# Kernel optimization log

Measured on AMD Instinct MI355X. Metric: run time of the kernel, lower is better.

Reference implementation:

```python
import jax, jax.numpy as jnp
import numpy as np

N_NODES = 100000
BN_EPS = 1e-5


def _linear_params(key, fan_in, fan_out):
    k1, k2 = jax.random.split(key)
    lim = 1.0 / np.sqrt(fan_in)
    W = jax.random.uniform(k1, (fan_in, fan_out), jnp.float32, -lim, lim)
    b = jax.random.uniform(k2, (fan_out,), jnp.float32, -lim, lim)
    return W, b


def setup_inputs() -> dict:
    key = jax.random.key(0)
    ks = jax.random.split(key, 24)
    in_ch, hid, tdim, L = 17, 64, 32, 2
    E = 1600000
    inp = {}
    inp["x"] = jax.random.normal(ks[0], (N_NODES, in_ch), jnp.float32)
    inp["edge_index"] = jax.random.randint(ks[1], (2, E), 0, N_NODES, jnp.int64)
    inp["edge_dts"] = jax.random.uniform(ks[2], (E,), jnp.float32) * 100.0
    inp["batch_size"] = 10000
    # TimeEncode params (learned, TGAT init)
    inp["basis_freq"] = jnp.asarray(1.0 / 10 ** np.linspace(0, 9, tdim), jnp.float32)
    inp["phase"] = jnp.zeros((tdim,), jnp.float32)
    # TMP edge MLP: in = 2*in_ch + tdim
    mi = 2 * in_ch + tdim
    inp["tmp_W1"], inp["tmp_b1"] = _linear_params(ks[3], mi, mi // 2)
    inp["tmp_W2"], inp["tmp_b2"] = _linear_params(ks[4], mi // 2, in_ch)
    inp["proj_W"], inp["proj_b"] = _linear_params(ks[5], in_ch, hid)
    # SMP layers (stacked over L)
    si = 2 * hid
    W1s, b1s, W2s, b2s = [], [], [], []
    for l in range(L):
        W1, b1 = _linear_params(ks[6 + 2 * l], si, si // 2)
        W2, b2 = _linear_params(ks[7 + 2 * l], si // 2, hid)
        W1s.append(W1); b1s.append(b1); W2s.append(W2); b2s.append(b2)
    inp["smp_W1"] = jnp.stack(W1s); inp["smp_b1"] = jnp.stack(b1s)
    inp["smp_W2"] = jnp.stack(W2s); inp["smp_b2"] = jnp.stack(b2s)
    inp["bn_gamma"] = jnp.ones((L, hid), jnp.float32)
    inp["bn_beta"] = jnp.zeros((L, hid), jnp.float32)
    # classifier head
    inp["clf_W1"], inp["clf_b1"] = _linear_params(ks[12], hid, hid)
    inp["clf_g1"] = jnp.ones((hid,), jnp.float32); inp["clf_bb1"] = jnp.zeros((hid,), jnp.float32)
    inp["clf_W2"], inp["clf_b2"] = _linear_params(ks[13], hid, hid // 2)
    inp["clf_g2"] = jnp.ones((hid // 2,), jnp.float32); inp["clf_bb2"] = jnp.zeros((hid // 2,), jnp.float32)
    inp["clf_W3"], inp["clf_b3"] = _linear_params(ks[14], hid // 2, 1)
    return inp


def _segment_mean(vals, idx, n):
    s = jax.ops.segment_sum(vals, idx, num_segments=n)
    c = jax.ops.segment_sum(jnp.ones((idx.shape[0], 1), vals.dtype), idx, num_segments=n)
    return s / jnp.maximum(c, 1.0)


def _bn(x, g, b):
    m = x.mean(0)
    v = x.var(0)
    return (x - m) * jax.lax.rsqrt(v + BN_EPS) * g + b


def reference(x, edge_index, edge_dts, batch_size, basis_freq, phase,
              tmp_W1, tmp_b1, tmp_W2, tmp_b2, proj_W, proj_b,
              smp_W1, smp_b1, smp_W2, smp_b2, bn_gamma, bn_beta,
              clf_W1, clf_b1, clf_g1, clf_bb1,
              clf_W2, clf_b2, clf_g2, clf_bb2, clf_W3, clf_b3):
    src, dst = edge_index[0], edge_index[1]  # x_j = x[src], x_i = x[dst]
    n = x.shape[0]
    # TimeEncode: cos(t * freq + phase)  -> [E, time_dim]
    rel = jnp.cos(edge_dts[:, None] * basis_freq + phase)
    # --- TMP conv (applied once) ---
    x_i = x[dst]
    m_in = jnp.concatenate([x_i, x[src], rel], axis=-1)
    p = jnp.tanh(jax.nn.relu(m_in @ tmp_W1 + tmp_b1) @ tmp_W2 + tmp_b2)
    msg = (2.0 * p - 1.0) * x_i  # (p - q) * x_i with q = 1 - p
    h = x + _segment_mean(msg, dst, n)
    # --- project to hidden ---
    h = h @ proj_W + proj_b
    # --- L SMP layers with BatchNorm + ReLU (dropout = eval/identity) ---
    L = smp_W1.shape[0]
    for l in range(L):
        h_i = h[dst]
        m_in = jnp.concatenate([h_i, h[src]], axis=-1)
        p = jnp.tanh(jax.nn.relu(m_in @ smp_W1[l] + smp_b1[l]) @ smp_W2[l] + smp_b2[l])
        h = h + _segment_mean((2.0 * p - 1.0) * h_i, dst, n)
        h = jax.nn.relu(_bn(h, bn_gamma[l], bn_beta[l]))
    # --- classifier on seed nodes ---
    z = h[:batch_size]
    z = jax.nn.relu(_bn(z @ clf_W1 + clf_b1, clf_g1, clf_bb1))
    z = jax.nn.relu(_bn(z @ clf_W2 + clf_b2, clf_g2, clf_bb2))
    return z @ clf_W3 + clf_b3  # [batch_size, 1] logits
```

## Files before the change

kernel.cpp:

```cpp
#include <hip/hip_runtime.h>
#include <hip/hip_bf16.h>


typedef float  f32x4 __attribute__((ext_vector_type(4)));
typedef short  s16x8 __attribute__((ext_vector_type(8)));

__device__ __forceinline__ float tanh_factor(float u) {
  float e = __expf(2.0f * u);
  return fmaf(-4.0f, __builtin_amdgcn_rcpf(e + 1.0f), 1.0f);
}

__device__ __forceinline__ void atomic_add_f32(float* p, float v) {
  unsafeAtomicAdd(p, v);
}

__device__ __forceinline__ unsigned short f2bf(float f) {
  __hip_bfloat16 b = __float2bfloat16(f);
  return *(unsigned short*)&b;
}
__device__ __forceinline__ float bf2f(unsigned short u) {
  unsigned int v = ((unsigned int)u) << 16;
  return *(float*)&v;
}

__global__ __launch_bounds__(256) void k_hist(
    const int* __restrict__ ei, int* __restrict__ cntI, int E)
{
  int e = blockIdx.x * 256 + threadIdx.x;
  if (e < E) atomicAdd(&cntI[__builtin_nontemporal_load(ei + E + e)], 1);
}

__global__ __launch_bounds__(256) void k_scan_block(
    const int* __restrict__ cntI, int* __restrict__ cursor,
    int* __restrict__ bsum, int N)
{
  __shared__ int s[256];
  const int t = threadIdx.x;
  int i = blockIdx.x * 256 + t;
  int v = (i < N) ? cntI[i] : 0;
  s[t] = v;
  for (int off = 1; off < 256; off <<= 1) {
    __syncthreads();
    int x = (t >= off) ? s[t - off] : 0;
    __syncthreads();
    s[t] += x;
  }
  __syncthreads();
  if (i < N) cursor[i] = s[t] - v;
  if (t == 255) bsum[blockIdx.x] = s[255];
}

__global__ __launch_bounds__(512) void k_scan_bsum(int* __restrict__ bsum, int nb)
{
  __shared__ int s[512];
  const int t = threadIdx.x;
  int v = (t < nb) ? bsum[t] : 0;
  s[t] = v;
  for (int off = 1; off < 512; off <<= 1) {
    __syncthreads();
    int x = (t >= off) ? s[t - off] : 0;
    __syncthreads();
    s[t] += x;
  }
  __syncthreads();
  if (t < nb) bsum[t] = s[t] - v;
}

__global__ __launch_bounds__(256) void k_expand_add(
    int* __restrict__ cursor, const int* __restrict__ bsum,
    const int* __restrict__ cntI, int* __restrict__ dstS, int N)
{
  int n = blockIdx.x * 256 + threadIdx.x;
  if (n >= N) return;
  int cur = cursor[n] + bsum[blockIdx.x];
  cursor[n] = cur;
  int c = cntI[n];
  for (int i = 0; i < c; i++) dstS[cur + i] = n;
}

__global__ __launch_bounds__(256) void k_scatter_x(
    const int* __restrict__ ei, const float* __restrict__ dts,
    int* __restrict__ cursor, int2* __restrict__ srcdtS, int E, int N)
{
  const int g  = blockIdx.x & 7;
  const int bi = blockIdx.x >> 3;
  const int nb = gridDim.x >> 3;
  const int lo = (int)(((long long)N * g) >> 3);
  const int hi = (int)(((long long)N * (g + 1)) >> 3);
  for (int e = bi * 256 + threadIdx.x; e < E; e += nb * 256) {
    int d = __builtin_nontemporal_load(ei + E + e);
    if (d >= lo && d < hi) {
      int s = __builtin_nontemporal_load(ei + e);
      float dt = __builtin_nontemporal_load(dts + e);
      int pos = atomicAdd(&cursor[d], 1);
      srcdtS[pos] = make_int2(s, __float_as_int(dt));
    }
  }
}

__global__ __launch_bounds__(256) void prep_all(
    const float* __restrict__ x, const float* __restrict__ tW1,
    const float* __restrict__ tW2, const float* __restrict__ sW1,
    const float* __restrict__ sW2, const float* __restrict__ cW1,
    const float* __restrict__ cW2, unsigned short* __restrict__ xb,
    unsigned short* __restrict__ W1t1, unsigned short* __restrict__ W2t1,
    unsigned short* __restrict__ W1t, unsigned short* __restrict__ W2t,
    unsigned short* __restrict__ cW1t, unsigned short* __restrict__ cW2t, int N)
{
  int i = blockIdx.x * 256 + threadIdx.x;
  int totalX = N * 24;
  for (int idx = i; idx < totalX; idx += gridDim.x * 256) {
    int n = idx / 24, c = idx - n * 24;
    xb[idx] = (c < 17) ? f2bf(x[n * 17 + c]) : (unsigned short)0;
  }
  if (i < 48 * 96) {
    int n = i / 96, k = i - n * 96;
    int src = (k < 17) ? k : (k >= 24 && k < 41) ? (k - 24 + 17)
            : (k >= 48 && k < 80) ? (k - 48 + 34) : -1;
    W1t1[i] = (n < 33 && src >= 0) ? f2bf(tW1[src * 33 + n]) : (unsigned short)0;
  }
  if (i < 32 * 64) {
    int n = i / 64, k = i - n * 64;
    W2t1[i] = (n < 17 && k < 33) ? f2bf(tW2[k * 17 + n]) : (unsigned short)0;
  }
  if (i < 2 * 64 * 128) {
    int l = i >> 13; int r = i & 8191; int n = r >> 7; int k = r & 127;
    W1t[i] = f2bf(sW1[((size_t)l * 128 + k) * 64 + n]);
  }
  if (i < 2 * 64 * 64) {
    int l = i >> 12; int r = i & 4095; int n = r >> 6; int k = r & 63;
    W2t[i] = f2bf(sW2[((size_t)l * 64 + k) * 64 + n]);
  }
  if (i < 64 * 64) {
    int c = i >> 6, k = i & 63;
    cW1t[i] = f2bf(cW1[k * 64 + c]);
  }
  if (i < 32 * 64) {
    int c = i >> 6, k = i & 63;
    cW2t[i] = f2bf(cW2[k * 32 + c]);
  }
}

__global__ __launch_bounds__(256, 3) void phase1_edge_mfma(
    const unsigned short* __restrict__ xb, const int* __restrict__ dstS,
    const int2* __restrict__ srcdtS, const float* __restrict__ freq,
    const float* __restrict__ phs,
    const unsigned short* __restrict__ W1t1, const float* __restrict__ b1,
    const unsigned short* __restrict__ W2t1, const float* __restrict__ b2,
    float* __restrict__ accum, int E, int nwt)
{
  __shared__ unsigned short sA[64][104];
  __shared__ unsigned short sHid[64][72];
  __shared__ float sRed[64][20];
  __shared__ int   sDst[64];

  const int t = threadIdx.x;
  const int wv = t >> 6, lane = t & 63, l16 = lane & 15, quad = lane >> 4;
  const int r0 = wv * 16;

  s16x8 w1f[3][3], w2f[2][2];
  float bias1[3], bias2[2];
#pragma unroll
  for (int cb = 0; cb < 3; cb++) {
    int n = cb * 16 + l16;
#pragma unroll
    for (int kb = 0; kb < 3; kb++)
      w1f[cb][kb] = *(const s16x8*)&W1t1[n * 96 + kb * 32 + quad * 8];
    bias1[cb] = (n < 33) ? b1[n] : 0.0f;
  }
#pragma unroll
  for (int cb = 0; cb < 2; cb++) {
    int n = cb * 16 + l16;
#pragma unroll
    for (int kb = 0; kb < 2; kb++)
      w2f[cb][kb] = *(const s16x8*)&W2t1[n * 64 + kb * 32 + quad * 8];
    bias2[cb] = (n < 17) ? b2[n] : 0.0f;
  }

  for (int i = lane; i < 16 * 28; i += 64) {
    int rr = r0 + i / 28, c = i % 28;
    int col = (c < 6) ? 18 + c : (c < 12) ? 42 + (c - 6) : 80 + (c - 12);
    sA[rr][col] = 0;
  }
  for (int i = lane; i < 256; i += 64)
    sHid[r0 + (i >> 4)][48 + (i & 15)] = 0;

  const int gw = blockIdx.x * 4 + wv;
  const int nw = gridDim.x * 4;

  const int e_loc = lane >> 2, q = lane & 3;
  const int rr = r0 + e_loc;

  int ndP = 0; uint4 xa0, xa1; unsigned int xa2 = 0; float dtP = 0.0f;
  auto issue = [&](int tt) {
    int er = (tt << 4) + e_loc; if (er >= E) er = E - 1;
    if (q < 2) {
      ndP = q ? srcdtS[er].x : dstS[er];
      const unsigned short* src = &xb[(size_t)ndP * 24];
      xa0 = *(const uint4*)&src[0];
      xa1 = *(const uint4*)&src[8];
      xa2 = *(const unsigned int*)&src[16];
    } else {
      dtP = __int_as_float(srcdtS[er].y);
    }
  };
  issue(gw < nwt ? gw : 0);

  for (int tile = gw; tile < nwt; tile += nw) {
    const int eb = tile << 4;

    if (q < 2) {
      if (!q) sDst[rr] = ndP;
      const int base = q ? 24 : 0;
      *(uint4*)&sA[rr][base]     = xa0;
      *(uint4*)&sA[rr][base + 8] = xa1;
      *(unsigned int*)&sA[rr][base + 16] = xa2;
    } else {
      const int k0 = (q == 2) ? 0 : 16;
      unsigned short tmp[16] __attribute__((aligned(16)));
#pragma unroll
      for (int j = 0; j < 16; j++)
        tmp[j] = f2bf(__cosf(fmaf(dtP, freq[k0 + j], phs[k0 + j])));
      *(uint4*)&sA[rr][48 + k0]     = *(const uint4*)&tmp[0];
      *(uint4*)&sA[rr][48 + k0 + 8] = *(const uint4*)&tmp[8];
    }

    { int nt = tile + nw; issue(nt < nwt ? nt : tile); }

    f32x4 a1[3];
#pragma unroll
    for (int cb = 0; cb < 3; cb++)
      a1[cb] = (f32x4){bias1[cb], bias1[cb], bias1[cb], bias1[cb]};
#pragma unroll
    for (int kb = 0; kb < 3; kb++) {
      s16x8 aF = *(const s16x8*)&sA[r0 + l16][kb * 32 + quad * 8];
#pragma unroll
      for (int cb = 0; cb < 3; cb++)
        a1[cb] = __builtin_amdgcn_mfma_f32_16x16x32_bf16(aF, w1f[cb][kb], a1[cb], 0, 0, 0);
    }
#pragma unroll
    for (int cb = 0; cb < 3; cb++)
#pragma unroll
      for (int reg = 0; reg < 4; reg++)
        sHid[r0 + quad * 4 + reg][cb * 16 + l16] = f2bf(fmaxf(a1[cb][reg], 0.0f));

    f32x4 a2[2];
#pragma unroll
    for (int cb = 0; cb < 2; cb++)
      a2[cb] = (f32x4){bias2[cb], bias2[cb], bias2[cb], bias2[cb]};
#pragma unroll
    for (int kb = 0; kb < 2; kb++) {
      s16x8 aF = *(const s16x8*)&sHid[r0 + l16][kb * 32 + quad * 8];
#pragma unroll
      for (int cb = 0; cb < 2; cb++)
        a2[cb] = __builtin_amdgcn_mfma_f32_16x16x32_bf16(aF, w2f[cb][kb], a2[cb], 0, 0, 0);
    }

#pragma unroll
    for (int reg = 0; reg < 4; reg++) {
      int row = r0 + quad * 4 + reg;
      bool ok = (eb + quad * 4 + reg < E);
      sRed[row][l16] = ok ? tanh_factor(a2[0][reg]) : 0.0f;
      if (l16 == 0) sRed[row][16] = ok ? tanh_factor(a2[1][reg]) : 0.0f;
    }

    if (lane < 17) {
      int col = lane;
      float run = 0.0f;
      int cur = __builtin_amdgcn_readfirstlane(sDst[r0]);
#pragma unroll
      for (int k = 0; k < 16; k++) {
        int d = __builtin_amdgcn_readfirstlane(sDst[r0 + k]);
        float v = sRed[r0 + k][col];
        if (d != cur) {
          atomic_add_f32(&accum[(size_t)cur * 17 + col], run);
          run = 0.0f; cur = d;
        }
        run += v;
      }
      atomic_add_f32(&accum[(size_t)cur * 17 + col], run);
    }
  }
}

__global__ __launch_bounds__(256) void phase1_node(
    const float* __restrict__ x, const float* __restrict__ acc1,
    const int* __restrict__ cntI, const float* __restrict__ Wp,
    const float* __restrict__ bp, float* __restrict__ h,
    float* __restrict__ acc2, int N)
{
  __shared__ float s0[4][20];
  const int t = threadIdx.x;
  const int nb = blockIdx.x << 2;
  if (t < 68) {
    int nl = t / 17, c = t % 17;
    int n = nb + nl;
    float v = 0.0f;
    if (n < N) {
      float cnt = fmaxf((float)cntI[n], 1.0f);
      v = x[n * 17 + c] * (1.0f + acc1[n * 17 + c] / cnt);
    }
    s0[nl][c] = v;
  }
  __syncthreads();
  int nl = t >> 6, j = t & 63;
  int n = nb + nl;
  if (n < N) {
    float acc = bp[j];
#pragma unroll
    for (int c = 0; c < 17; c++) acc = fmaf(s0[nl][c], Wp[c * 64 + j], acc);
    h[n * 64 + j] = acc;
    acc2[n * 64 + j] = 0.0f;
  }
}

template <bool DO_BN>
__global__ void prep_P(
    float* __restrict__ h, const unsigned short* __restrict__ W1t,
    const float* __restrict__ b1,
    const float* __restrict__ bns, const float* __restrict__ bnq,
    const float* __restrict__ gam, const float* __restrict__ bet, float invR,
    unsigned short* __restrict__ P1, unsigned short* __restrict__ P2, int N)
{
  __shared__ unsigned short sH[64][72];
  __shared__ float sM[64], sS[64], sB[64];
  const int t = threadIdx.x;
  const int wv = t >> 6, lane = t & 63, l16 = lane & 15, quad = lane >> 4;
  const int nb = blockIdx.x << 6;

  if (DO_BN) {
    if (t < 64) {
      float m = bns[t] * invR;
      float var = bnq[t] * invR - m * m;
      sM[t] = m;
      sS[t] = gam[t] * rsqrtf(var + 1e-5f);
      sB[t] = bet[t];
    }
    __syncthreads();
  }

#pragma unroll
  for (int i = 0; i < 4; i++) {
    int g = t + i * 256;
    int r = g >> 4, c4 = (g & 15) << 2;
    int n0 = nb + r;
    bool valid = (n0 < N);
    int n = valid ? n0 : N - 1;
    float4 v = *(const float4*)&h[(size_t)n * 64 + c4];
    if (DO_BN) {
      v.x = fmaxf(fmaf(v.x - sM[c4 + 0], sS[c4 + 0], sB[c4 + 0]), 0.0f);
      v.y = fmaxf(fmaf(v.y - sM[c4 + 1], sS[c4 + 1], sB[c4 + 1]), 0.0f);
      v.z = fmaxf(fmaf(v.z - sM[c4 + 2], sS[c4 + 2], sB[c4 + 2]), 0.0f);
      v.w = fmaxf(fmaf(v.w - sM[c4 + 3], sS[c4 + 3], sB[c4 + 3]), 0.0f);
      if (valid) *(float4*)&h[(size_t)n0 * 64 + c4] = v;
    }
    ushort4 o = { f2bf(v.x), f2bf(v.y), f2bf(v.z), f2bf(v.w) };
    *(ushort4*)&sH[r][c4] = o;
  }
  __syncthreads();

  const int n = nb + wv * 16 + l16;
#pragma unroll
  for (int half = 0; half < 2; half++) {
    f32x4 acc[4];
#pragma unroll
    for (int cb = 0; cb < 4; cb++) {
      if (half == 0) {
        float4 bv = *(const float4*)&b1[cb * 16 + quad * 4];
        acc[cb] = (f32x4){bv.x, bv.y, bv.z, bv.w};
      } else {
        acc[cb] = (f32x4){0.0f, 0.0f, 0.0f, 0.0f};
      }
    }
#pragma unroll
    for (int kb = 0; kb < 2; kb++) {
      s16x8 bF = *(const s16x8*)&sH[wv * 16 + l16][kb * 32 + quad * 8];
#pragma unroll
      for (int cb = 0; cb < 4; cb++) {
        s16x8 aF = *(const s16x8*)&W1t[(cb * 16 + l16) * 128 + half * 64 + kb * 32 + quad * 8];
        acc[cb] = __builtin_amdgcn_mfma_f32_16x16x32_bf16(aF, bF, acc[cb], 0, 0, 0);
      }
    }
    if (n < N) {
      unsigned short* P = half ? P2 : P1;
#pragma unroll
      for (int cb = 0; cb < 4; cb++) {
        ushort4 o = { f2bf(acc[cb][0]), f2bf(acc[cb][1]),
                      f2bf(acc[cb][2]), f2bf(acc[cb][3]) };
        *(ushort4*)&P[(size_t)n * 64 + cb * 16 + quad * 4] = o;
      }
    }
  }
}

__global__ __launch_bounds__(256, 4) void phase2_edge(
    const unsigned short* __restrict__ P1, const unsigned short* __restrict__ P2,
    const int* __restrict__ dstS, const int2* __restrict__ srcdtS,
    const unsigned short* __restrict__ W2t, const float* __restrict__ b2,
    float* __restrict__ accum, int E, int nwt)
{
  __shared__ unsigned short sA[64][136];
  __shared__ int sDst[64];
  float* sRedF = (float*)&sA[0][0];

  const int t = threadIdx.x;
  const int wv = t >> 6, lane = t & 63, l16 = lane & 15, quad = lane >> 4;
  const int r0 = wv * 16;

  s16x8 w2f[4][2];
  f32x4 bias2v[4];
#pragma unroll
  for (int cb = 0; cb < 4; cb++) {
#pragma unroll
    for (int kb = 0; kb < 2; kb++)
      w2f[cb][kb] = *(const s16x8*)&W2t[(cb * 16 + l16) * 64 + kb * 32 + quad * 8];
    float4 bv = *(const float4*)&b2[cb * 16 + quad * 4];
    bias2v[cb] = (f32x4){bv.x, bv.y, bv.z, bv.w};
  }

  const int gw = blockIdx.x * 4 + wv;
  const int nw = gridDim.x * 4;
  const int eRow = r0 + l16;

  const int e_loc = lane >> 2, q = lane & 3;
  const int rr = r0 + e_loc;
  const unsigned short* const Pb = (q < 2) ? P1 : P2;
  const int cb0 = q * 32;
  const size_t sub = (size_t)((q & 1) * 32);

  int ndP = 0; uint4 pA, pB, pC, pD;
  auto issue = [&](int tt) {
    int er = (tt << 4) + e_loc; if (er >= E) er = E - 1;
    ndP = (q < 2) ? dstS[er] : srcdtS[er].x;
    const unsigned short* src = Pb + (size_t)ndP * 64 + sub;
    pA = *(const uint4*)&src[0];
    pB = *(const uint4*)&src[8];
    pC = *(const uint4*)&src[16];
    pD = *(const uint4*)&src[24];
  };
  issue(gw < nwt ? gw : 0);

  for (int tile = gw; tile < nwt; tile += nw) {
    const int eb = tile << 4;

    if (q == 0) sDst[rr] = ndP;
    *(uint4*)&sA[rr][cb0]      = pA;
    *(uint4*)&sA[rr][cb0 + 8]  = pB;
    *(uint4*)&sA[rr][cb0 + 16] = pC;
    *(uint4*)&sA[rr][cb0 + 24] = pD;

    { int nt = tile + nw; issue(nt < nwt ? nt : tile); }

    s16x8 hidf[2];
#pragma unroll
    for (int kb = 0; kb < 2; kb++) {
      s16x8 x1 = *(const s16x8*)&sA[eRow][kb * 32 + quad * 8];
      s16x8 x2 = *(const s16x8*)&sA[eRow][64 + kb * 32 + quad * 8];
      s16x8 hf;
#pragma unroll
      for (int j = 0; j < 8; j++) {
        float a = bf2f((unsigned short)x1[j]);
        float b = bf2f((unsigned short)x2[j]);
        hf[j] = (short)f2bf(fmaxf(a + b, 0.0f));
      }
      hidf[kb] = hf;
    }

    f32x4 acc[4];
#pragma unroll
    for (int cb = 0; cb < 4; cb++) acc[cb] = bias2v[cb];
#pragma unroll
    for (int kb = 0; kb < 2; kb++)
#pragma unroll
      for (int cb = 0; cb < 4; cb++)
        acc[cb] = __builtin_amdgcn_mfma_f32_16x16x32_bf16(w2f[cb][kb], hidf[kb], acc[cb], 0, 0, 0);

    bool ok = (eb + l16 < E);
#pragma unroll
    for (int cb = 0; cb < 4; cb++) {
      f32x4 f;
#pragma unroll
      for (int reg = 0; reg < 4; reg++)
        f[reg] = ok ? tanh_factor(acc[cb][reg]) : 0.0f;
      *(f32x4*)&sRedF[eRow * 68 + cb * 16 + quad * 4] = f;
    }

    {
      float run = 0.0f;
      int cur = __builtin_amdgcn_readfirstlane(sDst[r0]);
#pragma unroll
      for (int k = 0; k < 16; k++) {
        int d = __builtin_amdgcn_readfirstlane(sDst[r0 + k]);
        float v = sRedF[(r0 + k) * 68 + lane];
        if (d != cur) {
          atomic_add_f32(&accum[(size_t)cur * 64 + lane], run);
          run = 0.0f; cur = d;
        }
        run += v;
      }
      atomic_add_f32(&accum[(size_t)cur * 64 + lane], run);
    }
  }
}

__global__ __launch_bounds__(256) void node_update_bn(
    float* __restrict__ h, float* __restrict__ accum,
    const int* __restrict__ cntI, float* __restrict__ bns,
    float* __restrict__ bnq, int N)
{
  const int t = threadIdx.x;
  float ls = 0.0f, lq = 0.0f;
  int total = N * 64;
  for (int idx = blockIdx.x * 256 + t; idx < total; idx += gridDim.x * 256) {
    int n = idx >> 6;
    float cnt = fmaxf((float)cntI[n], 1.0f);
    float v = h[idx] * (1.0f + accum[idx] / cnt);
    accum[idx] = 0.0f;
    h[idx] = v;
    ls += v; lq += v * v;
  }
  __shared__ float ss[256], sq[256];
  ss[t] = ls; sq[t] = lq;
  __syncthreads();
  if (t < 64) {
    float s = ss[t] + ss[t + 64] + ss[t + 128] + ss[t + 192];
    float q = sq[t] + sq[t + 64] + sq[t + 128] + sq[t + 192];
    atomic_add_f32(&bns[t], s);
    atomic_add_f32(&bnq[t], q);
  }
}

template <int NCB>
__global__ __launch_bounds__(256) void clf_mfma(
    const float* __restrict__ in, const unsigned short* __restrict__ Wt,
    const float* __restrict__ bias, float* __restrict__ z,
    float* __restrict__ bns, float* __restrict__ bnq,
    const float* __restrict__ ibns, const float* __restrict__ ibnq,
    const float* __restrict__ igam, const float* __restrict__ ibet,
    float iinvR, int rows)
{
  __shared__ unsigned short sIn[64][72];
  __shared__ float sM[64], sS[64], sB[64];
  const int t = threadIdx.x;
  const int wv = t >> 6, lane = t & 63, l16 = lane & 15, quad = lane >> 4;
  const int nb = blockIdx.x << 6;

  if (t < 64) {
    float m = ibns[t] * iinvR;
    float var = ibnq[t] * iinvR - m * m;
    sM[t] = m;
    sS[t] = igam[t] * rsqrtf(var + 1e-5f);
    sB[t] = ibet[t];
  }

  s16x8 wf[NCB][2];
  f32x4 bv[NCB];
#pragma unroll
  for (int cb = 0; cb < NCB; cb++) {
#pragma unroll
    for (int kb = 0; kb < 2; kb++)
      wf[cb][kb] = *(const s16x8*)&Wt[(cb * 16 + l16) * 64 + kb * 32 + quad * 8];
    float4 b4 = *(const float4*)&bias[cb * 16 + quad * 4];
    bv[cb] = (f32x4){b4.x, b4.y, b4.z, b4.w};
  }
  __syncthreads();

#pragma unroll
  for (int i = 0; i < 4; i++) {
    int g = t + i * 256;
    int r = g >> 4, c4 = (g & 15) << 2;
    int n = nb + r; if (n >= rows) n = rows - 1;
    float4 v = *(const float4*)&in[(size_t)n * 64 + c4];
    v.x = fmaxf(fmaf(v.x - sM[c4 + 0], sS[c4 + 0], sB[c4 + 0]), 0.0f);
    v.y = fmaxf(fmaf(v.y - sM[c4 + 1], sS[c4 + 1], sB[c4 + 1]), 0.0f);
    v.z = fmaxf(fmaf(v.z - sM[c4 + 2], sS[c4 + 2], sB[c4 + 2]), 0.0f);
    v.w = fmaxf(fmaf(v.w - sM[c4 + 3], sS[c4 + 3], sB[c4 + 3]), 0.0f);
    ushort4 o = { f2bf(v.x), f2bf(v.y), f2bf(v.z), f2bf(v.w) };
    *(ushort4*)&sIn[r][c4] = o;
  }
  __syncthreads();

  const int n = nb + wv * 16 + l16;
  const bool ok = (n < rows);
  f32x4 acc[NCB];
#pragma unroll
  for (int cb = 0; cb < NCB; cb++) acc[cb] = bv[cb];
#pragma unroll
  for (int kb = 0; kb < 2; kb++) {
    s16x8 bF = *(const s16x8*)&sIn[wv * 16 + l16][kb * 32 + quad * 8];
#pragma unroll
    for (int cb = 0; cb < NCB; cb++)
      acc[cb] = __builtin_amdgcn_mfma_f32_16x16x32_bf16(wf[cb][kb], bF, acc[cb], 0, 0, 0);
  }

#pragma unroll
  for (int cb = 0; cb < NCB; cb++) {
    if (ok)
      *(float4*)&z[(size_t)n * (NCB * 16) + cb * 16 + quad * 4] =
          make_float4(acc[cb][0], acc[cb][1], acc[cb][2], acc[cb][3]);
    f32x4 s, q;
#pragma unroll
    for (int reg = 0; reg < 4; reg++) {
      float v = ok ? acc[cb][reg] : 0.0f;
      s[reg] = v; q[reg] = v * v;
    }
#pragma unroll
    for (int m = 1; m < 16; m <<= 1) {
#pragma unroll
      for (int reg = 0; reg < 4; reg++) {
        s[reg] += __shfl_xor(s[reg], m);
        q[reg] += __shfl_xor(q[reg], m);
      }
    }
    if (l16 == 0) {
#pragma unroll
      for (int reg = 0; reg < 4; reg++) {
        int col = cb * 16 + quad * 4 + reg;
        atomic_add_f32(&bns[col], s[reg]);
        atomic_add_f32(&bnq[col], q[reg]);
      }
    }
  }
}

__global__ __launch_bounds__(256) void clf_final(
    const float* __restrict__ z2, const float* __restrict__ W3,
    const float* __restrict__ b3,
    const float* __restrict__ ibns, const float* __restrict__ ibnq,
    const float* __restrict__ igam, const float* __restrict__ ibet,
    float iinvR, float* __restrict__ out, int rows)
{
  __shared__ float sM[32], sS[32], sB[32];
  const int t = threadIdx.x;
  if (t < 32) {
    float m = ibns[t] * iinvR;
    float var = ibnq[t] * iinvR - m * m;
    sM[t] = m;
    sS[t] = igam[t] * rsqrtf(var + 1e-5f);
    sB[t] = ibet[t];
  }
  __syncthreads();
  int n = blockIdx.x * 256 + t;
  if (n >= rows) return;
  float acc = b3[0];
#pragma unroll
  for (int k = 0; k < 32; k++) {
    float v = fmaxf(fmaf(z2[n * 32 + k] - sM[k], sS[k], sB[k]), 0.0f);
    acc = fmaf(v, W3[k], acc);
  }
  out[n] = acc;
}

extern "C" void kernel_launch(void* const* d_in, const int* in_sizes, int n_in,
                              void* d_out, int out_size, void* d_ws, size_t ws_size,
                              hipStream_t stream)
{
  const float* x    = (const float*)d_in[0];
  const int*   ei   = (const int*)  d_in[1];
  const float* dts  = (const float*)d_in[2];
  const float* freq = (const float*)d_in[4];
  const float* phs  = (const float*)d_in[5];
  const float* tW1  = (const float*)d_in[6];
  const float* tb1  = (const float*)d_in[7];
  const float* tW2  = (const float*)d_in[8];
  const float* tb2  = (const float*)d_in[9];
  const float* pW   = (const float*)d_in[10];
  const float* pb   = (const float*)d_in[11];
  const float* sW1  = (const float*)d_in[12];
  const float* sb1  = (const float*)d_in[13];
  const float* sW2  = (const float*)d_in[14];
  const float* sb2  = (const float*)d_in[15];
  const float* bng  = (const float*)d_in[16];
  const float* bnb  = (const float*)d_in[17];
  const float* cW1  = (const float*)d_in[18];
  const float* cb1  = (const float*)d_in[19];
  const float* cg1  = (const float*)d_in[20];
  const float* cbb1 = (const float*)d_in[21];
  const float* cW2  = (const float*)d_in[22];
  const float* cb2  = (const float*)d_in[23];
  const float* cg2  = (const float*)d_in[24];
  const float* cbb2 = (const float*)d_in[25];
  const float* cW3  = (const float*)d_in[26];
  const float* cb3  = (const float*)d_in[27];
  float* out = (float*)d_out;

  const int N = in_sizes[0] / 17;
  const int E = in_sizes[1] / 2;
  const int B = out_size;

  char* base = (char*)d_ws;
  size_t off = 0;
  float* h    = (float*)(base + off); off += (size_t)N * 64 * 4;
  float* acc2 = (float*)(base + off); off += (size_t)N * 64 * 4;
  char*  uni  = base + off;           off += (size_t)N * 64 * 4;
  float* bnsAll = (float*)(base + off); off += 8 * 64 * 4;
  unsigned short* W1t = (unsigned short*)(base + off); off += 2 * 64 * 128 * 2;
  unsigned short* W2t = (unsigned short*)(base + off); off += 2 * 64 * 64 * 2;
  unsigned short* cW1t = (unsigned short*)(base + off); off += 64 * 64 * 2;
  unsigned short* cW2t = (unsigned short*)(base + off); off += 32 * 64 * 2;
  int* cntI   = (int*)(base + off); off += (size_t)N * 4;
  int* cursor = (int*)(base + off); off += (size_t)N * 4;
  int* bsum   = (int*)(base + off); off += 512 * 4;
  int* dstS   = (int*)(base + off); off += (size_t)E * 4;
  off = (off + 15) & ~(size_t)15;
  int2* srcdtS = (int2*)(base + off); off += (size_t)E * 8;
  size_t needed = off;
  if (ws_size < needed) return;

  float* acc1 = (float*)uni;
  unsigned short* xb   = (unsigned short*)(uni + (size_t)N * 17 * 4);
  unsigned short* W1t1 = xb + (size_t)N * 24;
  unsigned short* W2t1 = W1t1 + 48 * 96;
  unsigned short* P1 = (unsigned short*)uni;
  unsigned short* P2 = P1 + (size_t)N * 64;
  float* z1 = (float*)uni;
  float* z2 = z1 + (size_t)B * 64;

  const int nwt = (E + 15) / 16;
  const int NB = (N + 255) / 256;
  if (NB > 512) return;

  hipMemsetAsync(cntI, 0, (size_t)N * 4, stream);
  hipMemsetAsync(acc1, 0, (size_t)N * 17 * 4, stream);
  hipMemsetAsync(bnsAll, 0, 8 * 64 * 4, stream);

  k_hist<<<(E + 255) / 256, 256, 0, stream>>>(ei, cntI, E);
  k_scan_block<<<NB, 256, 0, stream>>>(cntI, cursor, bsum, N);
  k_scan_bsum<<<1, 512, 0, stream>>>(bsum, NB);
  k_expand_add<<<NB, 256, 0, stream>>>(cursor, bsum, cntI, dstS, N);
  k_scatter_x<<<1024, 256, 0, stream>>>(ei, dts, cursor, srcdtS, E, N);
  prep_all<<<(N * 24 + 255) / 256, 256, 0, stream>>>(
      x, tW1, tW2, sW1, sW2, cW1, cW2, xb, W1t1, W2t1, W1t, W2t, cW1t, cW2t, N);

  phase1_edge_mfma<<<768, 256, 0, stream>>>(
      xb, dstS, srcdtS, freq, phs, W1t1, tb1, W2t1, tb2, acc1, E, nwt);
  phase1_node<<<(N + 3) / 4, 256, 0, stream>>>(x, acc1, cntI, pW, pb, h, acc2, N);

  const int PB = (N + 63) / 64;
  prep_P<false><<<PB, 256, 0, stream>>>(
      h, W1t, sb1, nullptr, nullptr, nullptr, nullptr, 0.0f, P1, P2, N);
  phase2_edge<<<1024, 256, 0, stream>>>(
      P1, P2, dstS, srcdtS, W2t, sb2, acc2, E, nwt);
  node_update_bn<<<1024, 256, 0, stream>>>(h, acc2, cntI,
                                           bnsAll + 0, bnsAll + 64, N);
  prep_P<true><<<PB, 256, 0, stream>>>(
      h, W1t + (size_t)64 * 128, sb1 + 64, bnsAll + 0, bnsAll + 64,
      bng, bnb, 1.0f / (float)N, P1, P2, N);
  phase2_edge<<<1024, 256, 0, stream>>>(
      P1, P2, dstS, srcdtS, W2t + (size_t)64 * 64, sb2 + 64, acc2, E, nwt);
  node_update_bn<<<1024, 256, 0, stream>>>(h, acc2, cntI,
                                           bnsAll + 128, bnsAll + 192, N);

  const int CB = (B + 63) / 64;
  clf_mfma<4><<<CB, 256, 0, stream>>>(
      h, cW1t, cb1, z1, bnsAll + 256, bnsAll + 320,
      bnsAll + 128, bnsAll + 192, bng + 64, bnb + 64, 1.0f / (float)N, B);
  clf_mfma<2><<<CB, 256, 0, stream>>>(
      z1, cW2t, cb2, z2, bnsAll + 384, bnsAll + 448,
      bnsAll + 256, bnsAll + 320, cg1, cbb1, 1.0f / (float)B, B);
  clf_final<<<(B + 255) / 256, 256, 0, stream>>>(
      z2, cW3, cb3, bnsAll + 384, bnsAll + 448, cg2, cbb2,
      1.0f / (float)B, out, B);
}
```

Baseline: 826.1 us.

## Partition edge tiles into XCD-local contiguous ranges and spread time-encoding across lanes

Both edge kernels now give each group of blocks sharing blockIdx%8 (likely one XCD each under round-robin dispatch) a contiguous eighth of the dst-sorted edge tiles. The intent is that gathers and scatter atomics to nearby destination nodes stay in one XCD's L2. The first kernel also splits the 32 cosine time-encoding terms across all four lanes per edge (8 each) with freq/phase held in registers, instead of two lanes doing 16 each. Risks are load imbalance if gridDim is not a multiple of 8, and extra srcdt loads on every lane.

After: 814.1 us. No clear change (-1.5%).

```diff
diff --git a/kernel.cpp b/kernel.cpp
--- a/kernel.cpp
+++ b/kernel.cpp
@@ -157,6 +157,8 @@
   const int t = threadIdx.x;
   const int wv = t >> 6, lane = t & 63, l16 = lane & 15, quad = lane >> 4;
   const int r0 = wv * 16;
+  const int e_loc = lane >> 2, q = lane & 3;
+  const int rr = r0 + e_loc;
 
   s16x8 w1f[3][3], w2f[2][2];
   float bias1[3], bias2[2];
@@ -177,19 +179,26 @@
     bias2[cb] = (n < 17) ? b2[n] : 0.0f;
   }
 
+  float frq[8], phv[8];
+#pragma unroll
+  for (int j = 0; j < 8; j++) {
+    frq[j] = freq[q * 8 + j];
+    phv[j] = phs[q * 8 + j];
+  }
+
   for (int i = lane; i < 16 * 28; i += 64) {
-    int rr = r0 + i / 28, c = i % 28;
+    int rrz = r0 + i / 28, c = i % 28;
     int col = (c < 6) ? 18 + c : (c < 12) ? 42 + (c - 6) : 80 + (c - 12);
-    sA[rr][col] = 0;
+    sA[rrz][col] = 0;
   }
   for (int i = lane; i < 256; i += 64)
     sHid[r0 + (i >> 4)][48 + (i & 15)] = 0;
 
-  const int gw = blockIdx.x * 4 + wv;
-  const int nw = gridDim.x * 4;
-
-  const int e_loc = lane >> 2, q = lane & 3;
-  const int rr = r0 + e_loc;
+  const int g8   = blockIdx.x & 7;
+  const int tLo  = (int)(((long long)nwt * g8) >> 3);
+  const int tHi  = (int)(((long long)nwt * (g8 + 1)) >> 3);
+  const int wLoc = (blockIdx.x >> 3) * 4 + wv;
+  const int nwLoc = (gridDim.x >> 3) * 4;
 
   int ndP = 0; uint4 xa0, xa1; unsigned int xa2 = 0; float dtP = 0.0f;
   auto issue = [&](int tt) {
@@ -200,13 +209,15 @@
       xa0 = *(const uint4*)&src[0];
       xa1 = *(const uint4*)&src[8];
       xa2 = *(const unsigned int*)&src[16];
-    } else {
-      dtP = __int_as_float(srcdtS[er].y);
-    }
+    }
+    dtP = __int_as_float(srcdtS[er].y);
   };
-  issue(gw < nwt ? gw : 0);
-
-  for (int tile = gw; tile < nwt; tile += nw) {
+  {
+    int t0 = tLo + wLoc; if (t0 >= nwt) t0 = nwt - 1;
+    issue(t0);
+  }
+
+  for (int tile = tLo + wLoc; tile < tHi; tile += nwLoc) {
     const int eb = tile << 4;
 
     if (q < 2) {
@@ -215,17 +226,16 @@
       *(uint4*)&sA[rr][base]     = xa0;
       *(uint4*)&sA[rr][base + 8] = xa1;
       *(unsigned int*)&sA[rr][base + 16] = xa2;
-    } else {
-      const int k0 = (q == 2) ? 0 : 16;
-      unsigned short tmp[16] __attribute__((aligned(16)));
-#pragma unroll
-      for (int j = 0; j < 16; j++)
-        tmp[j] = f2bf(__cosf(fmaf(dtP, freq[k0 + j], phs[k0 + j])));
-      *(uint4*)&sA[rr][48 + k0]     = *(const uint4*)&tmp[0];
-      *(uint4*)&sA[rr][48 + k0 + 8] = *(const uint4*)&tmp[8];
-    }
-
-    { int nt = tile + nw; issue(nt < nwt ? nt : tile); }
+    }
+    {
+      unsigned short tmp[8] __attribute__((aligned(16)));
+#pragma unroll
+      for (int j = 0; j < 8; j++)
+        tmp[j] = f2bf(__cosf(fmaf(dtP, frq[j], phv[j])));
+      *(uint4*)&sA[rr][48 + q * 8] = *(const uint4*)&tmp[0];
+    }
+
+    { int nt = tile + nwLoc; issue(nt < tHi ? nt : tile); }
 
     f32x4 a1[3];
 #pragma unroll
@@ -418,8 +428,6 @@
     bias2v[cb] = (f32x4){bv.x, bv.y, bv.z, bv.w};
   }
 
-  const int gw = blockIdx.x * 4 + wv;
-  const int nw = gridDim.x * 4;
   const int eRow = r0 + l16;
 
   const int e_loc = lane >> 2, q = lane & 3;
@@ -427,6 +435,12 @@
   const unsigned short* const Pb = (q < 2) ? P1 : P2;
   const int cb0 = q * 32;
   const size_t sub = (size_t)((q & 1) * 32);
+
+  const int g8   = blockIdx.x & 7;
+  const int tLo  = (int)(((long long)nwt * g8) >> 3);
+  const int tHi  = (int)(((long long)nwt * (g8 + 1)) >> 3);
+  const int wLoc = (blockIdx.x >> 3) * 4 + wv;
+  const int nwLoc = (gridDim.x >> 3) * 4;
 
   int ndP = 0; uint4 pA, pB, pC, pD;
   auto issue = [&](int tt) {
@@ -438,9 +452,12 @@
     pC = *(const uint4*)&src[16];
     pD = *(const uint4*)&src[24];
   };
-  issue(gw < nwt ? gw : 0);
-
-  for (int tile = gw; tile < nwt; tile += nw) {
+  {
+    int t0 = tLo + wLoc; if (t0 >= nwt) t0 = nwt - 1;
+    issue(t0);
+  }
+
+  for (int tile = tLo + wLoc; tile < tHi; tile += nwLoc) {
     const int eb = tile << 4;
 
     if (q == 0) sDst[rr] = ndP;
@@ -449,7 +466,7 @@
     *(uint4*)&sA[rr][cb0 + 16] = pC;
     *(uint4*)&sA[rr][cb0 + 24] = pD;
 
-    { int nt = tile + nw; issue(nt < nwt ? nt : tile); }
+    { int nt = tile + nwLoc; issue(nt < tHi ? nt : tile); }
 
     s16x8 hidf[2];
 #pragma unroll
```
